# Kernel tuning notes

Hardware: AMD Instinct MI355X
Metric: run time of the kernel (lower is better)

## Reference

```python
import jax, jax.numpy as jnp
import numpy as np
import math

B, S, D = 16, 4096, 64

def setup_inputs() -> dict:
    key = jax.random.key(0)
    kq, kk, kv = jax.random.split(key, 3)
    query = jax.random.normal(kq, (B, S, D), dtype=jnp.float32)
    k_ = jax.random.normal(kk, (B, S, D), dtype=jnp.float32)
    value = jax.random.normal(kv, (B, S, D), dtype=jnp.float32)
    # causal mask: 1 = allowed, 0 = masked (set to -inf), broadcast over batch
    mask = jnp.tril(jnp.ones((S, S), dtype=jnp.int32))[None, :, :]
    return {"query": query, "key": k_, "value": value, "mask": mask, "key_dim": D}

def reference(query, key, value, mask, key_dim):
    # scores: [B, S, S] = Q @ K^T / sqrt(dk)
    scores = jnp.einsum('bqd,bkd->bqk', query, key) / math.sqrt(key_dim)
    scores = jnp.where(mask == 0, -jnp.inf, scores)
    attn = jax.nn.softmax(scores, axis=-1)
    return jnp.einsum('bqk,bkd->bqd', attn, value)
```

## Files before the change

### kernel.cpp

```cpp
#include <hip/hip_runtime.h>

typedef _Float16 half8 __attribute__((ext_vector_type(8)));
typedef __fp16 fp16x2 __attribute__((ext_vector_type(2)));
typedef float f32x4 __attribute__((ext_vector_type(4)));
typedef unsigned int uint32x2 __attribute__((ext_vector_type(2)));

union Frag { half8 v; unsigned int u32[4]; uint4 u4; };
union Pack4 { _Float16 h[4]; unsigned int u[2]; };
union H2U { fp16x2 h; unsigned int u; };

constexpr int S = 4096;
constexpr int D = 64;
constexpr int NB = 16;
constexpr int LTS = 72;

__device__ __forceinline__ float ex2(float x) {
#if __has_builtin(__builtin_amdgcn_exp2f)
    return __builtin_amdgcn_exp2f(x);
#else
    return exp2f(x);
#endif
}

__global__ __launch_bounds__(256)
void prep_kernel(const float* __restrict__ K, const float* __restrict__ V,
                 _Float16* __restrict__ K16, _Float16* __restrict__ VT) {
    __shared__ float tl[64 * 66];
    const int tid = threadIdx.x;
    const int s0 = blockIdx.x * 64;
    const int b  = blockIdx.y;
    const float* Kb = K + ((size_t)b * S + s0) * D;
    const float* Vb = V + ((size_t)b * S + s0) * D;
    _Float16* K16b = K16 + ((size_t)b * S + s0) * D;

    #pragma unroll
    for (int i = 0; i < 2; ++i) {
        int e8 = tid + 256 * i;
        float4 a = ((const float4*)Kb)[2 * e8];
        float4 c = ((const float4*)Kb)[2 * e8 + 1];
        Frag f;
        f.v[0]=(_Float16)a.x; f.v[1]=(_Float16)a.y; f.v[2]=(_Float16)a.z; f.v[3]=(_Float16)a.w;
        f.v[4]=(_Float16)c.x; f.v[5]=(_Float16)c.y; f.v[6]=(_Float16)c.z; f.v[7]=(_Float16)c.w;
        ((uint4*)K16b)[e8] = f.u4;
    }
    #pragma unroll
    for (int i = 0; i < 4; ++i) {
        int fi = tid + 256 * i;
        int r = fi >> 4, c4 = (fi & 15) << 2;
        float4 v = *(const float4*)(Vb + (size_t)r * D + c4);
        float2* p = (float2*)&tl[r * 66 + c4];
        p[0] = make_float2(v.x, v.y);
        p[1] = make_float2(v.z, v.w);
    }
    __syncthreads();
    _Float16* VTb = VT + (size_t)b * D * S;
    #pragma unroll
    for (int i = 0; i < 2; ++i) {
        int fi = tid + 256 * i;
        int d = fi >> 3, s8 = (fi & 7) << 3;
        Frag f;
        #pragma unroll
        for (int j = 0; j < 8; ++j) f.v[j] = (_Float16)tl[(s8 + j) * 66 + d];
        *(uint4*)(VTb + (size_t)d * S + s0 + s8) = f.u4;
    }
}

template <int SPLIT>
__device__ __forceinline__
void fattn_body(const float* __restrict__ Q, const _Float16* __restrict__ K16,
                const _Float16* __restrict__ VT16, float* __restrict__ Out,
                _Float16* __restrict__ OP, float* __restrict__ LP,
                int b, int J, int t0, int t1, int h) {
    __shared__ __align__(16) _Float16 kt[64 * LTS];
    __shared__ __align__(16) _Float16 vt[64 * LTS];

    const int tid  = threadIdx.x;
    const int lane = tid & 63;
    const int wave = tid >> 6;
    const int ln   = lane & 15;
    const int quad = lane >> 4;

    const float* Qb = Q + (size_t)b * S * D;
    const _Float16* Kb = K16 + (size_t)b * S * D;
    const _Float16* VTb = VT16 + (size_t)b * D * S;

    const float qscale = 0.125f * 1.44269504088896340736f;
    const int qrow_base = J * 128 + wave * 32;
    const int tw = (qrow_base + 31) >> 6;

    Frag qf[2][2];
    #pragma unroll
    for (int qg = 0; qg < 2; ++qg) {
        const float* qrow = Qb + (size_t)(qrow_base + qg * 16 + ln) * D + quad * 8;
        #pragma unroll
        for (int ks = 0; ks < 2; ++ks) {
            float4 a = *(const float4*)(qrow + ks * 32);
            float4 c = *(const float4*)(qrow + ks * 32 + 4);
            Frag f;
            f.v[0]=(_Float16)(a.x*qscale); f.v[1]=(_Float16)(a.y*qscale);
            f.v[2]=(_Float16)(a.z*qscale); f.v[3]=(_Float16)(a.w*qscale);
            f.v[4]=(_Float16)(c.x*qscale); f.v[5]=(_Float16)(c.y*qscale);
            f.v[6]=(_Float16)(c.z*qscale); f.v[7]=(_Float16)(c.w*qscale);
            qf[qg][ks] = f;
        }
    }

    f32x4 o[2][4] = {};
    float l_acc[2] = {0.f, 0.f};

    const int r0_ = tid >> 3,         c8_0 = (tid & 7) << 3;
    const int r1_ = (tid + 256) >> 3, c8_1 = ((tid + 256) & 7) << 3;
    uint4 pk0, pk1, pv0, pv1;
    auto issue = [&](int tt) {
        const int kk0 = tt * 64;
        pk0 = *(const uint4*)(Kb + (size_t)(kk0 + r0_) * D + c8_0);
        pv0 = *(const uint4*)(VTb + (size_t)r0_ * S + kk0 + c8_0);
        pk1 = *(const uint4*)(Kb + (size_t)(kk0 + r1_) * D + c8_1);
        pv1 = *(const uint4*)(VTb + (size_t)r1_ * S + kk0 + c8_1);
    };
    if (t0 < t1) issue(t0);

    for (int t = t0; t < t1; ++t) {
        const int k0 = t * 64;
        __syncthreads();
        *(uint4*)(kt + r0_ * LTS + c8_0) = pk0;
        *(uint4*)(vt + r0_ * LTS + c8_0) = pv0;
        *(uint4*)(kt + r1_ * LTS + c8_1) = pk1;
        *(uint4*)(vt + r1_ * LTS + c8_1) = pv1;
        __syncthreads();
        if (t + 1 < t1) issue(t + 1);

        #pragma unroll
        for (int ks = 0; ks < 2; ++ks) {
            unsigned w[2][2][2];
            #pragma unroll
            for (int cl = 0; cl < 2; ++cl) {
                const int ct = ks * 2 + cl;
                Frag kf0, kf1;
                kf0.u4 = *(const uint4*)(kt + (ct * 16 + ln) * LTS + quad * 8);
                kf1.u4 = *(const uint4*)(kt + (ct * 16 + ln) * LTS + 32 + quad * 8);
                #pragma unroll
                for (int qg = 0; qg < 2; ++qg) {
                    f32x4 acc = {0.f, 0.f, 0.f, 0.f};
                    acc = __builtin_amdgcn_mfma_f32_16x16x32_f16(kf0.v, qf[qg][0].v, acc, 0, 0, 0);
                    acc = __builtin_amdgcn_mfma_f32_16x16x32_f16(kf1.v, qf[qg][1].v, acc, 0, 0, 0);
                    if (t >= tw) {
                        int keyb = k0 + ct * 16 + quad * 4;
                        int qrow = qrow_base + qg * 16 + ln;
                        #pragma unroll
                        for (int r = 0; r < 4; ++r)
                            if (keyb + r > qrow) acc[r] = -1e30f;
                    }
                    float p0 = ex2(acc[0]), p1 = ex2(acc[1]);
                    float p2 = ex2(acc[2]), p3 = ex2(acc[3]);
                    l_acc[qg] += (p0 + p1) + (p2 + p3);
#if __has_builtin(__builtin_amdgcn_cvt_pkrtz)
                    H2U c0, c1;
                    c0.h = __builtin_amdgcn_cvt_pkrtz(p0, p1);
                    c1.h = __builtin_amdgcn_cvt_pkrtz(p2, p3);
                    w[qg][cl][0] = c0.u;
                    w[qg][cl][1] = c1.u;
#else
                    Pack4 pk;
                    pk.h[0] = (_Float16)p0; pk.h[1] = (_Float16)p1;
                    pk.h[2] = (_Float16)p2; pk.h[3] = (_Float16)p3;
                    w[qg][cl][0] = pk.u[0];
                    w[qg][cl][1] = pk.u[1];
#endif
                }
            }

            Frag pf[2];
            #pragma unroll
            for (int qg = 0; qg < 2; ++qg) {
                unsigned x0 = w[qg][0][0], y0 = w[qg][1][0];
                unsigned x1 = w[qg][0][1], y1 = w[qg][1][1];
#if __has_builtin(__builtin_amdgcn_permlane32_swap) && __has_builtin(__builtin_amdgcn_permlane16_swap)
                uint32x2 r;
                r = __builtin_amdgcn_permlane32_swap(x0, y0, false, false); x0 = r[0]; y0 = r[1];
                r = __builtin_amdgcn_permlane32_swap(x1, y1, false, false); x1 = r[0]; y1 = r[1];
                r = __builtin_amdgcn_permlane16_swap(x0, y0, false, false); x0 = r[0]; y0 = r[1];
                r = __builtin_amdgcn_permlane16_swap(x1, y1, false, false); x1 = r[0]; y1 = r[1];
#else
                asm volatile("s_nop 1\n\tv_permlane32_swap_b32 %0, %1\n\ts_nop 1"
                             : "+v"(x0), "+v"(y0));
                asm volatile("v_permlane32_swap_b32 %0, %1\n\ts_nop 1"
                             : "+v"(x1), "+v"(y1));
                asm volatile("v_permlane16_swap_b32 %0, %1\n\ts_nop 1"
                             : "+v"(x0), "+v"(y0));
                asm volatile("v_permlane16_swap_b32 %0, %1\n\ts_nop 1"
                             : "+v"(x1), "+v"(y1));
#endif
                pf[qg].u32[0] = x0; pf[qg].u32[1] = x1;
                pf[qg].u32[2] = y0; pf[qg].u32[3] = y1;
            }

            #pragma unroll
            for (int sub = 0; sub < 4; ++sub) {
                Frag vf;
                vf.u4 = *(const uint4*)(vt + (sub * 16 + ln) * LTS + ks * 32 + quad * 8);
                #pragma unroll
                for (int qg = 0; qg < 2; ++qg)
                    o[qg][sub] = __builtin_amdgcn_mfma_f32_16x16x32_f16(pf[qg].v, vf.v, o[qg][sub], 0, 0, 0);
            }
        }
    }

    float lf[2];
    #pragma unroll
    for (int qg = 0; qg < 2; ++qg) {
        float x = l_acc[qg];
        x += __shfl_xor(x, 16, 64);
        x += __shfl_xor(x, 32, 64);
        lf[qg] = x;
    }

    if (SPLIT) {
        _Float16* OPb = OP + (size_t)(((b * 32 + J) * 4 + h)) * 8192;
        float* LPb = LP + (size_t)(((b * 32 + J) * 4 + h)) * 128;
        #pragma unroll
        for (int qg = 0; qg < 2; ++qg) {
            if (quad == 0) LPb[wave * 32 + qg * 16 + ln] = lf[qg];
            #pragma unroll
            for (int r = 0; r < 4; ++r) {
                float lrow = __shfl(lf[qg], quad * 4 + r, 64);
                float inv = (lrow > 0.f) ? (1.0f / lrow) : 0.f;
                #pragma unroll
                for (int sub = 0; sub < 4; ++sub)
                    OPb[(wave * 32 + qg * 16 + quad * 4 + r) * 64 + sub * 16 + ln] =
                        (_Float16)(o[qg][sub][r] * inv);
            }
        }
    } else {
        float* Ob = Out + (size_t)b * S * D;
        #pragma unroll
        for (int qg = 0; qg < 2; ++qg) {
            #pragma unroll
            for (int r = 0; r < 4; ++r) {
                float lrow = __shfl(lf[qg], quad * 4 + r, 64);
                float inv = 1.0f / lrow;
                #pragma unroll
                for (int sub = 0; sub < 4; ++sub)
                    Ob[(size_t)(qrow_base + qg * 16 + quad * 4 + r) * D + sub * 16 + ln] =
                        o[qg][sub][r] * inv;
            }
        }
    }
}

__global__ __launch_bounds__(256, 4)
void fattn_split_kernel(const float* __restrict__ Q, const _Float16* __restrict__ K16,
                        const _Float16* __restrict__ VT16,
                        _Float16* __restrict__ OP, float* __restrict__ LP) {
    const int bx = blockIdx.x;
    const int J = 31 - (bx >> 6);
    const int h = (bx >> 4) & 3;
    const int b = bx & 15;
    const int n  = 2 * J + 2;
    const int t0 = (h * n) >> 2;
    const int t1 = ((h + 1) * n) >> 2;
    fattn_body<1>(Q, K16, VT16, nullptr, OP, LP, b, J, t0, t1, h);
}

__global__ __launch_bounds__(256, 4)
void fattn_kernel(const float* __restrict__ Q, const _Float16* __restrict__ K16,
                  const _Float16* __restrict__ VT16, float* __restrict__ Out) {
    const int bx = blockIdx.x;
    const int J = 31 - (bx >> 4);
    const int b = bx & 15;
    fattn_body<0>(Q, K16, VT16, Out, nullptr, nullptr, b, J, 0, 2 * J + 2, 0);
}

__global__ __launch_bounds__(256)
void reduce_kernel(const _Float16* __restrict__ OP, const float* __restrict__ LP,
                   float* __restrict__ Out) {
    const int rb = blockIdx.x;
    const int b  = rb & 15;
    const int J  = rb >> 4;
    const int tid = threadIdx.x;
    const _Float16* p = OP + (size_t)(b * 32 + J) * 4 * 8192;
    const float* l = LP + (size_t)(b * 32 + J) * 4 * 128;
    float* Ob = Out + (size_t)b * S * D + (size_t)J * 8192;
    #pragma unroll
    for (int i = 0; i < 4; ++i) {
        int e8 = tid + 256 * i;
        int q  = e8 >> 3;
        float lw[4], lsum = 0.f;
        #pragma unroll
        for (int hh = 0; hh < 4; ++hh) { lw[hh] = l[hh * 128 + q]; lsum += lw[hh]; }
        float inv = 1.0f / lsum;
        float acc[8] = {};
        #pragma unroll
        for (int hh = 0; hh < 4; ++hh) {
            half8 v = *(const half8*)(p + (size_t)hh * 8192 + e8 * 8);
            #pragma unroll
            for (int j = 0; j < 8; ++j) acc[j] += lw[hh] * (float)v[j];
        }
        float4 r0, r1;
        r0.x = acc[0]*inv; r0.y = acc[1]*inv; r0.z = acc[2]*inv; r0.w = acc[3]*inv;
        r1.x = acc[4]*inv; r1.y = acc[5]*inv; r1.z = acc[6]*inv; r1.w = acc[7]*inv;
        ((float4*)Ob)[2 * e8]     = r0;
        ((float4*)Ob)[2 * e8 + 1] = r1;
    }
}

extern "C" void kernel_launch(void* const* d_in, const int* in_sizes, int n_in,
                              void* d_out, int out_size, void* d_ws, size_t ws_size,
                              hipStream_t stream) {
    const float* Q = (const float*)d_in[0];
    const float* K = (const float*)d_in[1];
    const float* V = (const float*)d_in[2];
    float* O = (float*)d_out;

    const size_t prepBytes = (size_t)NB * S * D * 2;
    _Float16* K16  = (_Float16*)d_ws;
    _Float16* VT16 = (_Float16*)((char*)d_ws + prepBytes);

    const size_t opOff = 2 * prepBytes;
    const size_t opBytes = (size_t)NB * 32 * 4 * 8192 * 2;
    const size_t lpOff = opOff + opBytes;
    const size_t lpBytes = (size_t)NB * 32 * 4 * 128 * 4;
    const size_t need = lpOff + lpBytes;

    hipLaunchKernelGGL(prep_kernel, dim3(S / 64, NB), dim3(256), 0, stream, K, V, K16, VT16);

    if (ws_size >= need) {
        _Float16* OP = (_Float16*)((char*)d_ws + opOff);
        float* LP = (float*)((char*)d_ws + lpOff);
        hipLaunchKernelGGL(fattn_split_kernel, dim3(128 * NB), dim3(256), 0, stream,
                           Q, K16, VT16, OP, LP);
        hipLaunchKernelGGL(reduce_kernel, dim3(32 * NB), dim3(256), 0, stream, OP, LP, O);
    } else {
        hipLaunchKernelGGL(fattn_kernel, dim3(32 * NB), dim3(256), 0, stream, Q, K16, VT16, O);
    }
}
```

Before: 186.6 us.

## Double-buffer K/V shared-memory tiles to halve per-iteration barriers

Splits the K and V LDS tiles into two buffers. While one tile is being computed on, the next prefetched tile is written into the other buffer and the load for the tile after that is issued, so prefetching runs two tiles ahead. Each iteration now has one barrier instead of two, which cuts sync stalls and lets LDS writes overlap the MFMA work. In exchange, LDS use per block doubles, which may lower occupancy, and more registers stay live.

New measurement: 190.4 us. 1.02x slower.

```diff
diff --git a/kernel.cpp b/kernel.cpp
--- a/kernel.cpp
+++ b/kernel.cpp
@@ -71,8 +71,8 @@
                 const _Float16* __restrict__ VT16, float* __restrict__ Out,
                 _Float16* __restrict__ OP, float* __restrict__ LP,
                 int b, int J, int t0, int t1, int h) {
-    __shared__ __align__(16) _Float16 kt[64 * LTS];
-    __shared__ __align__(16) _Float16 vt[64 * LTS];
+    __shared__ __align__(16) _Float16 kt[2][64 * LTS];
+    __shared__ __align__(16) _Float16 vt[2][64 * LTS];
 
     const int tid  = threadIdx.x;
     const int lane = tid & 63;
@@ -118,17 +118,30 @@
         pk1 = *(const uint4*)(Kb + (size_t)(kk0 + r1_) * D + c8_1);
         pv1 = *(const uint4*)(VTb + (size_t)r1_ * S + kk0 + c8_1);
     };
-    if (t0 < t1) issue(t0);
+    auto stage = [&](_Float16* ktp, _Float16* vtp) {
+        *(uint4*)(ktp + r0_ * LTS + c8_0) = pk0;
+        *(uint4*)(vtp + r0_ * LTS + c8_0) = pv0;
+        *(uint4*)(ktp + r1_ * LTS + c8_1) = pk1;
+        *(uint4*)(vtp + r1_ * LTS + c8_1) = pv1;
+    };
+
+    if (t0 < t1) {
+        issue(t0);
+        stage(kt[0], vt[0]);
+        if (t0 + 1 < t1) issue(t0 + 1);
+        __syncthreads();
+    }
 
     for (int t = t0; t < t1; ++t) {
         const int k0 = t * 64;
-        __syncthreads();
-        *(uint4*)(kt + r0_ * LTS + c8_0) = pk0;
-        *(uint4*)(vt + r0_ * LTS + c8_0) = pv0;
-        *(uint4*)(kt + r1_ * LTS + c8_1) = pk1;
-        *(uint4*)(vt + r1_ * LTS + c8_1) = pv1;
-        __syncthreads();
-        if (t + 1 < t1) issue(t + 1);
+        const int p  = (t - t0) & 1;
+        const _Float16* ktp = kt[p];
+        const _Float16* vtp = vt[p];
+
+        if (t + 1 < t1) {
+            stage(kt[p ^ 1], vt[p ^ 1]);
+            if (t + 2 < t1) issue(t + 2);
+        }
 
         #pragma unroll
         for (int ks = 0; ks < 2; ++ks) {
@@ -137,8 +150,8 @@
             for (int cl = 0; cl < 2; ++cl) {
                 const int ct = ks * 2 + cl;
                 Frag kf0, kf1;
-                kf0.u4 = *(const uint4*)(kt + (ct * 16 + ln) * LTS + quad * 8);
-                kf1.u4 = *(const uint4*)(kt + (ct * 16 + ln) * LTS + 32 + quad * 8);
+                kf0.u4 = *(const uint4*)(ktp + (ct * 16 + ln) * LTS + quad * 8);
+                kf1.u4 = *(const uint4*)(ktp + (ct * 16 + ln) * LTS + 32 + quad * 8);
                 #pragma unroll
                 for (int qg = 0; qg < 2; ++qg) {
                     f32x4 acc = {0.f, 0.f, 0.f, 0.f};
@@ -198,12 +211,14 @@
             #pragma unroll
             for (int sub = 0; sub < 4; ++sub) {
                 Frag vf;
-                vf.u4 = *(const uint4*)(vt + (sub * 16 + ln) * LTS + ks * 32 + quad * 8);
+                vf.u4 = *(const uint4*)(vtp + (sub * 16 + ln) * LTS + ks * 32 + quad * 8);
                 #pragma unroll
                 for (int qg = 0; qg < 2; ++qg)
                     o[qg][sub] = __builtin_amdgcn_mfma_f32_16x16x32_f16(pf[qg].v, vf.v, o[qg][sub], 0, 0, 0);
             }
         }
+
+        __syncthreads();
     }
 
     float lf[2];
```
